# Performance work log

Measured on AMD Instinct MI355X. Metric: run time of the kernel, lower is better.

## Reference

```python
import jax, jax.numpy as jnp
import numpy as np

DIM = 768
HIDDEN = 4 * DIM          # shared expert hidden
NUM_EXPERTS = 8
TOPK = 2
D_LOW = DIM // 4          # 192


def setup_inputs() -> dict:
    key = jax.random.key(0)
    ks = jax.random.split(key, 8)
    B, C, H, W = 8, DIM, 32, 32
    x = jax.random.normal(ks[0], (B, C, H, W), dtype=jnp.float32)
    # shared expert (1x1 convs == per-pixel linear)
    w1 = jax.random.normal(ks[1], (HIDDEN, DIM), dtype=jnp.float32) * 0.02
    b1 = jnp.zeros((HIDDEN,), dtype=jnp.float32)
    w2 = jax.random.normal(ks[2], (DIM, HIDDEN), dtype=jnp.float32) * 0.02
    b2 = jnp.zeros((DIM,), dtype=jnp.float32)
    # router params (torch Linear weight layout [out, in])
    w_down = jax.random.normal(ks[3], (NUM_EXPERTS * D_LOW, DIM), dtype=jnp.float32) * 0.02
    router_w = jax.random.normal(ks[4], (1, D_LOW), dtype=jnp.float32) * 0.02
    w_up = jax.random.normal(ks[5], (NUM_EXPERTS, D_LOW, DIM), dtype=jnp.float32) * 0.02
    return {"x": x, "w1": w1, "b1": b1, "w2": w2, "b2": b2,
            "w_down": w_down, "router_w": router_w, "w_up": w_up}


def _gelu(v):
    # torch nn.GELU default = exact erf variant
    return jax.nn.gelu(v, approximate=False)


def reference(x, w1, b1, w2, b2, w_down, router_w, w_up):
    B, C, H, W = x.shape
    # ---- shared expert: conv1x1 -> GELU -> conv1x1 ----
    h = jnp.einsum('bchw,oc->bohw', x, w1) + b1[None, :, None, None]
    shared = jnp.einsum('bohw,co->bchw', _gelu(h), w2) + b2[None, :, None, None]
    # ---- AoE router over tokens ----
    N = H * W
    x_flat = x.reshape(B, C, N).transpose(0, 2, 1).reshape(B * N, C)  # [T, C]
    feats = (x_flat @ w_down.T).reshape(-1, NUM_EXPERTS, D_LOW)       # [T, E, d_low]
    logits = jnp.einsum('ted,d->te', feats, router_w[0])              # [T, E]
    probs = jax.nn.softmax(logits, axis=-1)
    topk_w, topk_i = jax.lax.top_k(probs, TOPK)                       # [T, k]
    topk_w = topk_w / jnp.sum(topk_w, axis=-1, keepdims=True)
    sel = jnp.take_along_axis(feats, topk_i[:, :, None], axis=1)      # [T, k, d_low]
    act = _gelu(sel)
    sel_w_up = w_up[topk_i]                                           # [T, k, d_low, C]
    expert_out = jnp.einsum('tkd,tkdm->tkm', act, sel_w_up)           # [T, k, C]
    weighted = jnp.sum(expert_out * topk_w[:, :, None], axis=1)       # [T, C]
    # aux load-balance loss
    mean_prob = jnp.mean(probs, axis=0)
    one_hot = jnp.sum(jax.nn.one_hot(topk_i, NUM_EXPERTS, dtype=probs.dtype), axis=1)
    mean_load = jnp.mean(one_hot, axis=0)
    aux_loss = NUM_EXPERTS * jnp.sum(mean_prob * mean_load)
    aoe = weighted.reshape(B, N, C).transpose(0, 2, 1).reshape(B, C, H, W)
    return x + shared + aoe, aux_loss
```

## Files before the change

kernel.cpp:

```cpp
#include <hip/hip_runtime.h>
#include <cstdint>
#include <cmath>

#define DIM   768
#define HID   3072
#define NEXP  8
#define DLOW  192
#define NPB   1024
#define NTOK  8192
#define KD    1536
#define KCAT  4608

typedef unsigned short ushort_t;
typedef short   short8  __attribute__((ext_vector_type(8)));
typedef float   float4v __attribute__((ext_vector_type(4)));

__device__ inline ushort_t f2b(float f) {
    union { float f; unsigned int i; } v; v.f = f;
    unsigned int x = v.i;
    return (ushort_t)((x + 0x7fffu + ((x >> 16) & 1u)) >> 16);
}
__device__ inline float b2f(ushort_t u) {
    union { unsigned int i; float f; } v; v.i = ((unsigned int)u) << 16; return v.f;
}
__device__ inline float gelu_fast(float x) {
    const float z = 1.5957691216057308f * x * __builtin_fmaf(0.044715f * x, x, 1.0f);
    return x * __builtin_amdgcn_rcpf(1.0f + __expf(-z));
}

__device__ __forceinline__ void async_ld16(const ushort_t* g, ushort_t* l) {
    __builtin_amdgcn_global_load_lds(
        (const __attribute__((address_space(1))) void*)g,
        (__attribute__((address_space(3))) void*)l,
        16, 0, 0);
}

__global__ __launch_bounds__(512)
void gemm_in(const ushort_t* __restrict__ A, const ushort_t* __restrict__ B,
             ushort_t* __restrict__ Cb, const float* __restrict__ bias,
             const int* __restrict__ tokE, const float* __restrict__ tokW,
             const float* __restrict__ accbuf, float* __restrict__ outAux,
             int m_base)
{
    __shared__ __align__(16) ushort_t As[256 * 64];
    __shared__ __align__(16) ushort_t Bs[128 * 64];

    const int tid  = threadIdx.x;
    const int lane = tid & 63;
    const int wave = tid >> 6;
    const int quad = lane >> 4;
    const int l16  = lane & 15;
    const int wm   = (wave >> 1) * 64;
    const int wn   = (wave & 1) * 64;

    const int nwg = gridDim.x * gridDim.y;
    const int bid = blockIdx.y * gridDim.x + blockIdx.x;
    const int swz = (bid & 7) * (nwg >> 3) + (bid >> 3);
    const int m0  = (swz / gridDim.x) * 256;
    const int n0  = (swz % gridDim.x) * 128;

    float4v acc[4][4];
#pragma unroll
    for (int i = 0; i < 4; i++)
#pragma unroll
        for (int j = 0; j < 4; j++) acc[i][j] = (float4v)0.0f;

    const ushort_t* ga[4]; ushort_t* la[4];
#pragma unroll
    for (int j = 0; j < 4; j++) {
        const int f = j * 512 + tid;
        const int mm = f >> 3;
        const int gs = ((f & 7) ^ (mm & 7)) * 8;
        ga[j] = A + (size_t)(m0 + mm) * DIM + gs;
        la[j] = &As[f * 8];
    }
    const ushort_t* gb[2]; ushort_t* lb[2];
#pragma unroll
    for (int j = 0; j < 2; j++) {
        const int f = j * 512 + tid;
        const int mm = f >> 3;
        const int gs = ((f & 7) ^ (mm & 7)) * 8;
        gb[j] = B + (size_t)(n0 + mm) * DIM + gs;
        lb[j] = &Bs[f * 8];
    }

    const ushort_t* pa[2][4]; const ushort_t* pb[2][4];
#pragma unroll
    for (int kh = 0; kh < 2; kh++)
#pragma unroll
        for (int i = 0; i < 4; i++) {
            const int ra = wm + i * 16 + l16;
            pa[kh][i] = &As[ra * 64 + (((quad + 4 * kh) ^ (ra & 7)) * 8)];
            const int rb = wn + i * 16 + l16;
            pb[kh][i] = &Bs[rb * 64 + (((quad + 4 * kh) ^ (rb & 7)) * 8)];
        }

    for (int k0 = 0; k0 < DIM; k0 += 64) {
        __syncthreads();
#pragma unroll
        for (int j = 0; j < 4; j++) async_ld16(ga[j] + k0, la[j]);
#pragma unroll
        for (int j = 0; j < 2; j++) async_ld16(gb[j] + k0, lb[j]);
        __syncthreads();
#pragma unroll
        for (int kh = 0; kh < 2; kh++) {
            short8 af[4], bv[4];
#pragma unroll
            for (int i = 0; i < 4; i++) af[i] = *(const short8*)pa[kh][i];
#pragma unroll
            for (int i = 0; i < 4; i++) bv[i] = *(const short8*)pb[kh][i];
#pragma unroll
            for (int im = 0; im < 4; im++)
#pragma unroll
                for (int in = 0; in < 4; in++)
                    acc[im][in] = __builtin_amdgcn_mfma_f32_16x16x32_bf16(
                        af[im], bv[in], acc[im][in], 0, 0, 0);
        }
    }

    if (n0 < HID) {
#pragma unroll
        for (int in = 0; in < 4; in++) {
            const int col = n0 + wn + in * 16 + l16;
            const float bvv = bias[col];
#pragma unroll
            for (int im = 0; im < 4; im++) {
                const int rowl = m0 + wm + im * 16 + quad * 4;
#pragma unroll
                for (int r = 0; r < 4; r++)
                    Cb[(size_t)(rowl + r) * KCAT + col] =
                        f2b(gelu_fast(acc[im][in][r] + bvv));
            }
        }
        if (m_base == 0 && blockIdx.x == 0 && blockIdx.y == 0 && tid == 0) {
            float aux = 0.0f;
            for (int e = 0; e < 8; e++) aux += accbuf[e] * accbuf[8 + e];
            outAux[0] = aux * 8.0f / ((float)NTOK * (float)NTOK);
        }
    } else {
        int eidx[4];
#pragma unroll
        for (int in = 0; in < 4; in++)
            eidx[in] = (n0 + wn + in * 16 - HID) / DLOW;
#pragma unroll
        for (int im = 0; im < 4; im++) {
            const int rowl = m0 + wm + im * 16 + quad * 4;
#pragma unroll
            for (int r = 0; r < 4; r++) {
                const int g = m_base + rowl + r;
                const int e0 = tokE[2 * g], e1 = tokE[2 * g + 1];
                const float w0 = tokW[2 * g], w1 = tokW[2 * g + 1];
#pragma unroll
                for (int in = 0; in < 4; in++) {
                    const int col = n0 + wn + in * 16 + l16;
                    const float m = (eidx[in] == e0) ? w0
                                  : ((eidx[in] == e1) ? w1 : 0.0f);
                    Cb[(size_t)(rowl + r) * KCAT + col] =
                        f2b(gelu_fast(acc[im][in][r]) * m);
                }
            }
        }
    }
}

__global__ __launch_bounds__(256)
void gemm_out(const ushort_t* __restrict__ A, const ushort_t* __restrict__ B,
              float* __restrict__ out, const float* __restrict__ bias,
              const float* __restrict__ X, int m_base)
{
    __shared__ __align__(16) ushort_t As[128 * 64];
    __shared__ __align__(16) ushort_t Bs[96 * 64];

    const int tid  = threadIdx.x;
    const int lane = tid & 63;
    const int wave = tid >> 6;
    const int quad = lane >> 4;
    const int l16  = lane & 15;
    const int wm   = (wave >> 1) * 64;
    const int wn   = (wave & 1) * 48;

    const int nwg = gridDim.x * gridDim.y;
    const int bid = blockIdx.y * gridDim.x + blockIdx.x;
    const int swz = (bid & 7) * (nwg >> 3) + (bid >> 3);
    const int m0  = (swz / gridDim.x) * 128;
    const int n0  = (swz % gridDim.x) * 96;

    float4v acc[4][3];
#pragma unroll
    for (int i = 0; i < 4; i++)
#pragma unroll
        for (int j = 0; j < 3; j++) acc[i][j] = (float4v)0.0f;

    const ushort_t* ga[4]; ushort_t* la[4];
#pragma unroll
    for (int j = 0; j < 4; j++) {
        const int f = j * 256 + tid;
        const int mm = f >> 3;
        const int gs = ((f & 7) ^ (mm & 7)) * 8;
        ga[j] = A + (size_t)(m0 + mm) * KCAT + gs;
        la[j] = &As[f * 8];
    }
    const ushort_t* gb[3]; ushort_t* lb[3];
#pragma unroll
    for (int j = 0; j < 3; j++) {
        const int f = j * 256 + tid;
        const int mm = f >> 3;
        const int gs = ((f & 7) ^ (mm & 7)) * 8;
        gb[j] = B + (size_t)(n0 + mm) * KCAT + gs;
        lb[j] = &Bs[f * 8];
    }

    const ushort_t* pa[2][4]; const ushort_t* pb[2][3];
#pragma unroll
    for (int kh = 0; kh < 2; kh++) {
#pragma unroll
        for (int i = 0; i < 4; i++) {
            const int ra = wm + i * 16 + l16;
            pa[kh][i] = &As[ra * 64 + (((quad + 4 * kh) ^ (ra & 7)) * 8)];
        }
#pragma unroll
        for (int i = 0; i < 3; i++) {
            const int rb = wn + i * 16 + l16;
            pb[kh][i] = &Bs[rb * 64 + (((quad + 4 * kh) ^ (rb & 7)) * 8)];
        }
    }

    for (int k0 = 0; k0 < KCAT; k0 += 64) {
        __syncthreads();
#pragma unroll
        for (int j = 0; j < 4; j++) async_ld16(ga[j] + k0, la[j]);
#pragma unroll
        for (int j = 0; j < 3; j++) async_ld16(gb[j] + k0, lb[j]);
        __syncthreads();
#pragma unroll
        for (int kh = 0; kh < 2; kh++) {
            short8 af[4], bv[3];
#pragma unroll
            for (int i = 0; i < 4; i++) af[i] = *(const short8*)pa[kh][i];
#pragma unroll
            for (int i = 0; i < 3; i++) bv[i] = *(const short8*)pb[kh][i];
#pragma unroll
            for (int im = 0; im < 4; im++)
#pragma unroll
                for (int in = 0; in < 3; in++)
                    acc[im][in] = __builtin_amdgcn_mfma_f32_16x16x32_bf16(
                        af[im], bv[in], acc[im][in], 0, 0, 0);
        }
    }

#pragma unroll
    for (int in = 0; in < 3; in++) {
        const int col = n0 + wn + in * 16 + l16;
        const float bvv = bias[col];
#pragma unroll
        for (int im = 0; im < 4; im++) {
            const int grow = m_base + m0 + wm + im * 16 + quad * 4;
            const int bb = grow >> 10, nn = grow & 1023;
            const size_t base = ((size_t)bb * DIM + col) * NPB + nn;
            const float4 xv = *(const float4*)(X + base);
            float4 v;
            v.x = acc[im][in][0] + bvv + xv.x;
            v.y = acc[im][in][1] + bvv + xv.y;
            v.z = acc[im][in][2] + bvv + xv.z;
            v.w = acc[im][in][3] + bvv + xv.w;
            *(float4*)(out + base) = v;
        }
    }
}

__global__ void transpose_x_cvt(const float* __restrict__ x, ushort_t* __restrict__ XT)
{
    __shared__ ushort_t tile[32][33];
    const int tx = threadIdx.x, ty = threadIdx.y;
    const int n0 = blockIdx.x * 32, c0 = blockIdx.y * 32, b = blockIdx.z;
#pragma unroll
    for (int j = 0; j < 4; j++)
        tile[ty + 8 * j][tx] = f2b(x[((size_t)b * DIM + c0 + ty + 8 * j) * NPB + n0 + tx]);
    __syncthreads();
#pragma unroll
    for (int j = 0; j < 4; j++)
        XT[((size_t)b * NPB + n0 + ty + 8 * j) * DIM + c0 + tx] = tile[tx][ty + 8 * j];
}

__global__ void transpose_wup_cat(const float* __restrict__ src, ushort_t* __restrict__ Wcat)
{
    __shared__ ushort_t tile[32][33];
    const int tx = threadIdx.x, ty = threadIdx.y;
    const int c0 = blockIdx.x * 32, k0 = blockIdx.y * 32;
#pragma unroll
    for (int j = 0; j < 4; j++)
        tile[ty + 8 * j][tx] = f2b(src[(size_t)(k0 + ty + 8 * j) * DIM + c0 + tx]);
    __syncthreads();
#pragma unroll
    for (int j = 0; j < 4; j++)
        Wcat[(size_t)(c0 + ty + 8 * j) * KCAT + HID + k0 + tx] = tile[tx][ty + 8 * j];
}

#define NB_W2  (DIM * HID / 4 / 256)
#define NB_WIN (KCAT * DIM / 4 / 256)
__global__ void cvt_weights(const float* __restrict__ w2, const float* __restrict__ w1,
                            const float* __restrict__ wdn,
                            ushort_t* __restrict__ Wcat, ushort_t* __restrict__ Win)
{
    const int blk = blockIdx.x;
    if (blk < NB_W2) {
        const int i = blk * 256 + threadIdx.x;
        const int c = i / (HID / 4), h = (i % (HID / 4)) * 4;
        const float4 v = *(const float4*)(w2 + (size_t)c * HID + h);
        uint2 p;
        p.x = (unsigned)f2b(v.x) | ((unsigned)f2b(v.y) << 16);
        p.y = (unsigned)f2b(v.z) | ((unsigned)f2b(v.w) << 16);
        *(uint2*)(Wcat + (size_t)c * KCAT + h) = p;
    } else {
        const int i = (blk - NB_W2) * 256 + threadIdx.x;
        const int n1 = HID * DIM / 4;
        const float4 v = (i < n1) ? ((const float4*)w1)[i]
                                  : ((const float4*)wdn)[i - n1];
        uint2 p;
        p.x = (unsigned)f2b(v.x) | ((unsigned)f2b(v.y) << 16);
        p.y = (unsigned)f2b(v.z) | ((unsigned)f2b(v.w) << 16);
        ((uint2*)Win)[i] = p;
    }
}

__global__ __launch_bounds__(256)
void weff_kernel(const float* __restrict__ wdn, const float* __restrict__ rw,
                 float* __restrict__ Weff)
{
    const int idx = blockIdx.x * 256 + threadIdx.x;
    const int e = idx / DIM, c = idx % DIM;
    float s = 0.0f;
    for (int d = 0; d < DLOW; d++)
        s += wdn[(size_t)(e * DLOW + d) * DIM + c] * rw[d];
    Weff[idx] = s;
}

__global__ __launch_bounds__(256)
void router_kernel(const float* __restrict__ x, const float* __restrict__ Weff,
                   int* __restrict__ tokE, float* __restrict__ tokW,
                   float* __restrict__ accbuf)
{
    __shared__ float sW[NEXP * DIM];
    __shared__ float sAcc[16];
    const int tid = threadIdx.x;
    for (int i = tid; i < NEXP * DIM; i += 256) sW[i] = Weff[i];
    if (tid < 16) sAcc[tid] = 0.0f;
    __syncthreads();

    const int t = blockIdx.x * 256 + tid;
    const int b = t >> 10, n = t & 1023;
    const float* xb = x + (size_t)b * DIM * NPB + n;

    float lg[8];
#pragma unroll
    for (int e = 0; e < 8; e++) lg[e] = 0.0f;
    for (int c = 0; c < DIM; c++) {
        const float xv = xb[(size_t)c * NPB];
#pragma unroll
        for (int e = 0; e < 8; e++) lg[e] += xv * sW[e * DIM + c];
    }

    float mx = lg[0];
#pragma unroll
    for (int e = 1; e < 8; e++) mx = fmaxf(mx, lg[e]);
    float pr[8], s = 0.0f;
#pragma unroll
    for (int e = 0; e < 8; e++) { pr[e] = expf(lg[e] - mx); s += pr[e]; }
    const float inv = 1.0f / s;
#pragma unroll
    for (int e = 0; e < 8; e++) pr[e] *= inv;
    int e0 = 0;
#pragma unroll
    for (int e = 1; e < 8; e++) if (pr[e] > pr[e0]) e0 = e;
    int e1 = (e0 == 0) ? 1 : 0;
#pragma unroll
    for (int e = 0; e < 8; e++) if (e != e0 && pr[e] > pr[e1]) e1 = e;
    const float wsum = pr[e0] + pr[e1];
    tokE[2 * t + 0] = e0;  tokE[2 * t + 1] = e1;
    tokW[2 * t + 0] = pr[e0] / wsum;  tokW[2 * t + 1] = pr[e1] / wsum;

#pragma unroll
    for (int e = 0; e < 8; e++) atomicAdd(&sAcc[e], pr[e]);
    atomicAdd(&sAcc[8 + e0], 1.0f);
    atomicAdd(&sAcc[8 + e1], 1.0f);
    __syncthreads();
    if (tid < 16) atomicAdd(&accbuf[tid], sAcc[tid]);
}

extern "C" void kernel_launch(void* const* d_in, const int* in_sizes, int n_in,
                              void* d_out, int out_size, void* d_ws, size_t ws_size,
                              hipStream_t stream)
{
    (void)in_sizes; (void)n_in; (void)out_size;

    const float* x   = (const float*)d_in[0];
    const float* w1  = (const float*)d_in[1];
    const float* b1  = (const float*)d_in[2];
    const float* w2  = (const float*)d_in[3];
    const float* b2  = (const float*)d_in[4];
    const float* wdn = (const float*)d_in[5];
    const float* rw  = (const float*)d_in[6];
    const float* wup = (const float*)d_in[7];
    float* out = (float*)d_out;

    char* ws = (char*)d_ws;
    size_t off = 0;
    ushort_t* XTbf = (ushort_t*)(ws + off); off += (size_t)NTOK * DIM * 2;
    ushort_t* Win  = (ushort_t*)(ws + off); off += (size_t)KCAT * DIM * 2;
    ushort_t* Wcat = (ushort_t*)(ws + off); off += (size_t)DIM * KCAT * 2;
    float*    Weff = (float*)  (ws + off);  off += (size_t)NEXP * DIM * 4;
    int*      tokE = (int*)    (ws + off);  off += (size_t)NTOK * 2 * 4;
    float*    tokW = (float*)  (ws + off);  off += (size_t)NTOK * 2 * 4;
    float*    accb = (float*)  (ws + off);  off += 256;

    int chunk = NTOK / 4;
    if      (ws_size >= off + (size_t)NTOK * KCAT * 2)       chunk = NTOK;
    else if (ws_size >= off + (size_t)(NTOK / 2) * KCAT * 2) chunk = NTOK / 2;
    ushort_t* HU = (ushort_t*)(ws + off);

    const dim3 tb(32, 8);
    transpose_x_cvt  <<<dim3(32, 24, 8), tb, 0, stream>>>(x, XTbf);
    transpose_wup_cat<<<dim3(24, 48),    tb, 0, stream>>>(wup, Wcat);
    cvt_weights<<<NB_W2 + NB_WIN, 256, 0, stream>>>(w2, w1, wdn, Wcat, Win);
    weff_kernel<<<NEXP * DIM / 256, 256, 0, stream>>>(wdn, rw, Weff);

    hipMemsetAsync(accb, 0, 64, stream);
    router_kernel<<<NTOK / 256, 256, 0, stream>>>(x, Weff, tokE, tokW, accb);

    for (int c = 0; c < NTOK / chunk; c++) {
        const ushort_t* Ax = XTbf + (size_t)c * chunk * DIM;
        const int m_base = c * chunk;
        gemm_in<<<dim3(KCAT / 128, chunk / 256), 512, 0, stream>>>(
            Ax, Win, HU, b1, tokE, tokW, accb, out + (size_t)NTOK * DIM, m_base);
        gemm_out<<<dim3(DIM / 96, chunk / 128), 256, 0, stream>>>(
            HU, Wcat, out, b2, x, m_base);
    }
}
```

Baseline: 329.9 us.

## Double-buffer gemm_out with wider N tile; shrink router/weff blocks

gemm_out now uses a 128x192 tile with two LDS buffers, so the async load of the next K slice overlaps the MFMA work on the current one, and the block swizzle is remapped. The aim is to hide global-load latency and raise arithmetic intensity per block, at the cost of more accumulator registers (launch bounds set to one block), more LDS and fewer blocks (4x64). Separately, weff_kernel and router_kernel drop to 64-thread blocks to spread the small router work over more CUs. Each router block still loads the full 24 KB Weff table into shared memory, so that staging traffic grows fourfold.

```diff
diff --git a/kernel.cpp b/kernel.cpp
--- a/kernel.cpp
+++ b/kernel.cpp
@@ -163,13 +163,13 @@
     }
 }
 
-__global__ __launch_bounds__(256)
+__global__ __launch_bounds__(256, 1)
 void gemm_out(const ushort_t* __restrict__ A, const ushort_t* __restrict__ B,
               float* __restrict__ out, const float* __restrict__ bias,
               const float* __restrict__ X, int m_base)
 {
-    __shared__ __align__(16) ushort_t As[128 * 64];
-    __shared__ __align__(16) ushort_t Bs[96 * 64];
+    __shared__ __align__(16) ushort_t As[2 * 128 * 64];
+    __shared__ __align__(16) ushort_t Bs[2 * 192 * 64];
 
     const int tid  = threadIdx.x;
     const int lane = tid & 63;
@@ -177,40 +177,43 @@
     const int quad = lane >> 4;
     const int l16  = lane & 15;
     const int wm   = (wave >> 1) * 64;
-    const int wn   = (wave & 1) * 48;
-
-    const int nwg = gridDim.x * gridDim.y;
+    const int wn   = (wave & 1) * 96;
+
+    const int mt  = gridDim.y;
+    const int nwg = gridDim.x * mt;
     const int bid = blockIdx.y * gridDim.x + blockIdx.x;
-    const int swz = (bid & 7) * (nwg >> 3) + (bid >> 3);
-    const int m0  = (swz / gridDim.x) * 128;
-    const int n0  = (swz % gridDim.x) * 96;
-
-    float4v acc[4][3];
+    const int s   = (bid & 7) * (nwg >> 3) + (bid >> 3);
+    const int m0  = (s % mt) * 128;
+    const int n0  = (s / mt) * 192;
+
+    float4v acc[4][6];
 #pragma unroll
     for (int i = 0; i < 4; i++)
 #pragma unroll
-        for (int j = 0; j < 3; j++) acc[i][j] = (float4v)0.0f;
-
-    const ushort_t* ga[4]; ushort_t* la[4];
+        for (int j = 0; j < 6; j++) acc[i][j] = (float4v)0.0f;
+
+    const ushort_t* ga[4]; ushort_t* la0[4]; ushort_t* la1[4];
 #pragma unroll
     for (int j = 0; j < 4; j++) {
         const int f = j * 256 + tid;
         const int mm = f >> 3;
         const int gs = ((f & 7) ^ (mm & 7)) * 8;
-        ga[j] = A + (size_t)(m0 + mm) * KCAT + gs;
-        la[j] = &As[f * 8];
-    }
-    const ushort_t* gb[3]; ushort_t* lb[3];
-#pragma unroll
-    for (int j = 0; j < 3; j++) {
+        ga[j]  = A + (size_t)(m0 + mm) * KCAT + gs;
+        la0[j] = &As[f * 8];
+        la1[j] = &As[128 * 64 + f * 8];
+    }
+    const ushort_t* gb[6]; ushort_t* lb0[6]; ushort_t* lb1[6];
+#pragma unroll
+    for (int j = 0; j < 6; j++) {
         const int f = j * 256 + tid;
         const int mm = f >> 3;
         const int gs = ((f & 7) ^ (mm & 7)) * 8;
-        gb[j] = B + (size_t)(n0 + mm) * KCAT + gs;
-        lb[j] = &Bs[f * 8];
-    }
-
-    const ushort_t* pa[2][4]; const ushort_t* pb[2][3];
+        gb[j]  = B + (size_t)(n0 + mm) * KCAT + gs;
+        lb0[j] = &Bs[f * 8];
+        lb1[j] = &Bs[192 * 64 + f * 8];
+    }
+
+    const ushort_t* pa[2][4]; const ushort_t* pb[2][6];
 #pragma unroll
     for (int kh = 0; kh < 2; kh++) {
 #pragma unroll
@@ -219,37 +222,49 @@
             pa[kh][i] = &As[ra * 64 + (((quad + 4 * kh) ^ (ra & 7)) * 8)];
         }
 #pragma unroll
-        for (int i = 0; i < 3; i++) {
+        for (int i = 0; i < 6; i++) {
             const int rb = wn + i * 16 + l16;
             pb[kh][i] = &Bs[rb * 64 + (((quad + 4 * kh) ^ (rb & 7)) * 8)];
         }
     }
 
-    for (int k0 = 0; k0 < KCAT; k0 += 64) {
+#define STAGE_OUT(k0, la, lb) do {                                          \
+    _Pragma("unroll")                                                       \
+    for (int j = 0; j < 4; j++) async_ld16(ga[j] + (k0), la[j]);            \
+    _Pragma("unroll")                                                       \
+    for (int j = 0; j < 6; j++) async_ld16(gb[j] + (k0), lb[j]); } while (0)
+
+#define COMPUTE_OUT(AOFS, BOFS) do {                                        \
+    _Pragma("unroll")                                                       \
+    for (int kh = 0; kh < 2; kh++) {                                        \
+        short8 af[4], bv[6];                                                \
+        _Pragma("unroll")                                                   \
+        for (int i = 0; i < 4; i++)                                         \
+            af[i] = *(const short8*)(pa[kh][i] + (AOFS));                   \
+        _Pragma("unroll")                                                   \
+        for (int i = 0; i < 6; i++)                                         \
+            bv[i] = *(const short8*)(pb[kh][i] + (BOFS));                   \
+        _Pragma("unroll")                                                   \
+        for (int im = 0; im < 4; im++)                                      \
+            _Pragma("unroll")                                               \
+            for (int in = 0; in < 6; in++)                                  \
+                acc[im][in] = __builtin_amdgcn_mfma_f32_16x16x32_bf16(      \
+                    af[im], bv[in], acc[im][in], 0, 0, 0);                  \
+    } } while (0)
+
+    STAGE_OUT(0, la0, lb0);
+    __syncthreads();
+    for (int t = 0; t < KCAT / 64; t += 2) {
+        STAGE_OUT((t + 1) * 64, la1, lb1);
+        COMPUTE_OUT(0, 0);
         __syncthreads();
-#pragma unroll
-        for (int j = 0; j < 4; j++) async_ld16(ga[j] + k0, la[j]);
-#pragma unroll
-        for (int j = 0; j < 3; j++) async_ld16(gb[j] + k0, lb[j]);
+        if (t + 2 < KCAT / 64) STAGE_OUT((t + 2) * 64, la0, lb0);
+        COMPUTE_OUT(128 * 64, 192 * 64);
         __syncthreads();
-#pragma unroll
-        for (int kh = 0; kh < 2; kh++) {
-            short8 af[4], bv[3];
-#pragma unroll
-            for (int i = 0; i < 4; i++) af[i] = *(const short8*)pa[kh][i];
-#pragma unroll
-            for (int i = 0; i < 3; i++) bv[i] = *(const short8*)pb[kh][i];
-#pragma unroll
-            for (int im = 0; im < 4; im++)
-#pragma unroll
-                for (int in = 0; in < 3; in++)
-                    acc[im][in] = __builtin_amdgcn_mfma_f32_16x16x32_bf16(
-                        af[im], bv[in], acc[im][in], 0, 0, 0);
-        }
-    }
-
-#pragma unroll
-    for (int in = 0; in < 3; in++) {
+    }
+
+#pragma unroll
+    for (int in = 0; in < 6; in++) {
         const int col = n0 + wn + in * 16 + l16;
         const float bvv = bias[col];
 #pragma unroll
@@ -266,6 +281,8 @@
             *(float4*)(out + base) = v;
         }
     }
+#undef STAGE_OUT
+#undef COMPUTE_OUT
 }
 
 __global__ void transpose_x_cvt(const float* __restrict__ x, ushort_t* __restrict__ XT)
@@ -323,11 +340,11 @@
     }
 }
 
-__global__ __launch_bounds__(256)
+__global__ __launch_bounds__(64)
 void weff_kernel(const float* __restrict__ wdn, const float* __restrict__ rw,
                  float* __restrict__ Weff)
 {
-    const int idx = blockIdx.x * 256 + threadIdx.x;
+    const int idx = blockIdx.x * 64 + threadIdx.x;
     const int e = idx / DIM, c = idx % DIM;
     float s = 0.0f;
     for (int d = 0; d < DLOW; d++)
@@ -335,7 +352,7 @@
     Weff[idx] = s;
 }
 
-__global__ __launch_bounds__(256)
+__global__ __launch_bounds__(64)
 void router_kernel(const float* __restrict__ x, const float* __restrict__ Weff,
                    int* __restrict__ tokE, float* __restrict__ tokW,
                    float* __restrict__ accbuf)
@@ -343,11 +360,11 @@
     __shared__ float sW[NEXP * DIM];
     __shared__ float sAcc[16];
     const int tid = threadIdx.x;
-    for (int i = tid; i < NEXP * DIM; i += 256) sW[i] = Weff[i];
+    for (int i = tid; i < NEXP * DIM; i += 64) sW[i] = Weff[i];
     if (tid < 16) sAcc[tid] = 0.0f;
     __syncthreads();
 
-    const int t = blockIdx.x * 256 + tid;
+    const int t = blockIdx.x * 64 + tid;
     const int b = t >> 10, n = t & 1023;
     const float* xb = x + (size_t)b * DIM * NPB + n;
 
@@ -422,17 +439,17 @@
     transpose_x_cvt  <<<dim3(32, 24, 8), tb, 0, stream>>>(x, XTbf);
     transpose_wup_cat<<<dim3(24, 48),    tb, 0, stream>>>(wup, Wcat);
     cvt_weights<<<NB_W2 + NB_WIN, 256, 0, stream>>>(w2, w1, wdn, Wcat, Win);
-    weff_kernel<<<NEXP * DIM / 256, 256, 0, stream>>>(wdn, rw, Weff);
+    weff_kernel<<<NEXP * DIM / 64, 64, 0, stream>>>(wdn, rw, Weff);
 
     hipMemsetAsync(accb, 0, 64, stream);
-    router_kernel<<<NTOK / 256, 256, 0, stream>>>(x, Weff, tokE, tokW, accb);
+    router_kernel<<<NTOK / 64, 64, 0, stream>>>(x, Weff, tokE, tokW, accb);
 
     for (int c = 0; c < NTOK / chunk; c++) {
         const ushort_t* Ax = XTbf + (size_t)c * chunk * DIM;
         const int m_base = c * chunk;
         gemm_in<<<dim3(KCAT / 128, chunk / 256), 512, 0, stream>>>(
             Ax, Win, HU, b1, tokE, tokW, accb, out + (size_t)NTOK * DIM, m_base);
-        gemm_out<<<dim3(DIM / 96, chunk / 128), 256, 0, stream>>>(
+        gemm_out<<<dim3(DIM / 192, chunk / 128), 256, 0, stream>>>(
             HU, Wcat, out, b2, x, m_base);
     }
 }
```

Result: slower. 362.7 us (+9.9%).
